# Kernel optimization log

Measured on AMD Instinct MI355X. Metric: run time of the kernel, lower is better.

The kernel has to match this reference:

```python
import jax, jax.numpy as jnp
import numpy as np

D = 512
H = 8
B, S = 4, 2048


def _layernorm(x, g, b, eps=1e-6):
    m = jnp.mean(x, axis=-1, keepdims=True)
    v = jnp.mean(jnp.square(x - m), axis=-1, keepdims=True)
    return (x - m) * jax.lax.rsqrt(v + eps) * g + b


def setup_inputs() -> dict:
    key = jax.random.key(0)
    ks = jax.random.split(key, 8)
    w = 1.0 / np.sqrt(D)  # glorot-ish scale so softmax doesn't saturate
    return {
        "x": jax.random.normal(ks[0], (B, S, D), dtype=jnp.float32),
        "Q": jax.random.normal(ks[1], (H, D, D), dtype=jnp.float32) * w,
        "K": jax.random.normal(ks[2], (H, D, D), dtype=jnp.float32) * w,
        "g1": jnp.ones((D,), jnp.float32),
        "beta1": jnp.zeros((D,), jnp.float32),
        "Wp": jax.random.normal(ks[3], (H * D, D), dtype=jnp.float32) / np.sqrt(H * D),
        "bp": jnp.zeros((D,), jnp.float32),
        "g2": jnp.ones((D,), jnp.float32),
        "beta2": jnp.zeros((D,), jnp.float32),
        "W1": jax.random.normal(ks[4], (D, 4 * D), dtype=jnp.float32) * w,
        "b1": jnp.zeros((4 * D,), jnp.float32),
        "W2": jax.random.normal(ks[5], (4 * D, D), dtype=jnp.float32) / np.sqrt(4 * D),
        "b2": jnp.zeros((D,), jnp.float32),
    }


def reference(x, Q, K, g1, beta1, Wp, bp, g2, beta2, W1, b1, W2, b2):
    # layernorm1
    xn = _layernorm(x, g1, beta1)  # [B,S,D]
    # per-head attention, batched over heads via einsum
    Qx = jnp.einsum("bsd,hde->hbse", xn, Q)  # [H,B,S,D]
    Kx = jnp.einsum("bsd,hde->hbse", xn, K)  # [H,B,S,D]
    scale = 1.0 / jnp.sqrt(jnp.float32(D))
    A = jnp.einsum("hbse,hbte->hbst", Qx, Kx) * scale  # [H,B,S,S]
    A = jax.nn.softmax(A, axis=-1)
    head = jnp.einsum("hbst,btd->hbsd", A, xn) + xn  # per-head residual
    # concat heads along last axis: order h0,h1,... -> [B,S,H*D]
    cat = jnp.transpose(head, (1, 2, 0, 3)).reshape(x.shape[0], x.shape[1], -1)
    # projection
    y = cat @ Wp + bp  # [B,S,D]
    # layernorm2
    y = _layernorm(y, g2, beta2)
    # MLP with residual, exact gelu (keras default)
    h = jax.nn.gelu(y @ W1 + b1, approximate=False)
    h = jax.nn.gelu(h @ W2 + b2, approximate=False)
    return y + h
```

## Files before the change

kernel.cpp:

```cpp
#include <hip/hip_runtime.h>

using u16 = unsigned short;
typedef u16 u16x8 __attribute__((ext_vector_type(8)));
typedef __bf16 bf16x8 __attribute__((ext_vector_type(8)));
typedef float f32x4 __attribute__((ext_vector_type(4)));

__device__ __forceinline__ u16 f2bf(float f) {
  unsigned u = __builtin_bit_cast(unsigned, f);
  u += 0x7fffu + ((u >> 16) & 1u);
  return (u16)(u >> 16);
}
__device__ __forceinline__ float bf2f(u16 h) {
  unsigned u = ((unsigned)h) << 16;
  return __builtin_bit_cast(float, u);
}
__device__ __forceinline__ f32x4 mfma16(u16x8 a, u16x8 b, f32x4 c) {
  return __builtin_amdgcn_mfma_f32_16x16x32_bf16(
      __builtin_bit_cast(bf16x8, a), __builtin_bit_cast(bf16x8, b), c, 0, 0, 0);
}
__device__ __forceinline__ float gelu_f(float v) {
  return 0.5f * v * (1.0f + erff(v * 0.70710678118654752f));
}
__device__ __forceinline__ void gll16(const u16* g, u16* l) {
  __builtin_amdgcn_global_load_lds(
      (const __attribute__((address_space(1))) unsigned*)g,
      (__attribute__((address_space(3))) unsigned*)l, 16, 0, 0);
}

__global__ void cast_kernel(const float* __restrict__ in, u16* __restrict__ out,
                            float scale) {
  const size_t i = ((size_t)blockIdx.x * 256 + threadIdx.x) * 4;
  float4 v = *(const float4*)(in + i);
  out[i] = f2bf(v.x * scale);
  out[i + 1] = f2bf(v.y * scale);
  out[i + 2] = f2bf(v.z * scale);
  out[i + 3] = f2bf(v.w * scale);
}

__device__ __forceinline__ float loadf(const float* p) { return *p; }
__device__ __forceinline__ float loadf(const u16* p) { return bf2f(*p); }

template <typename T>
__global__ void tcast_kernel(const T* __restrict__ in, u16* __restrict__ out, int R, int C,
                             float scale) {
  __shared__ float tile[32][33];
  const T* ip = in + (size_t)blockIdx.z * R * C;
  u16* op = out + (size_t)blockIdx.z * R * C;
  int c0 = blockIdx.x * 32, r0 = blockIdx.y * 32;
  int tx = threadIdx.x, ty = threadIdx.y;
#pragma unroll
  for (int i = 0; i < 32; i += 8)
    tile[ty + i][tx] = loadf(ip + (size_t)(r0 + ty + i) * C + (c0 + tx));
  __syncthreads();
#pragma unroll
  for (int i = 0; i < 32; i += 8)
    op[(size_t)(c0 + ty + i) * R + (r0 + tx)] = f2bf(tile[tx][ty + i] * scale);
}

__global__ void vtile_kernel(const u16* __restrict__ in, u16* __restrict__ out) {
  __shared__ u16 tile[32][33];
  const int b = blockIdx.z;
  const int d0 = blockIdx.x * 32, t0 = blockIdx.y * 32;
  const int tx = threadIdx.x, ty = threadIdx.y;
  const u16* ip = in + (size_t)b * 2048 * 512;
#pragma unroll
  for (int i = 0; i < 32; i += 8)
    tile[ty + i][tx] = ip[(size_t)(t0 + ty + i) * 512 + d0 + tx];
  __syncthreads();
  u16* op = out + ((size_t)b * 64 + (t0 >> 5)) * 16384;
#pragma unroll
  for (int i = 0; i < 32; i += 8) {
    const int d = d0 + ty + i;
    op[(size_t)(tx >> 3) * 4096 + (size_t)d * 8 + (tx & 7)] = tile[tx][ty + i];
  }
}

__global__ __launch_bounds__(256) void ln_kernel(
    const float* __restrict__ x, const float* __restrict__ x2,
    const float* __restrict__ g, const float* __restrict__ b,
    u16* __restrict__ obf, float* __restrict__ of32) {
  const int D = 512;
  int row = blockIdx.x;
  const float* xr = x + (size_t)row * D;
  float2 v = ((const float2*)xr)[threadIdx.x];
  if (x2 != nullptr) {
    float2 v2 = ((const float2*)(x2 + (size_t)row * D))[threadIdx.x];
    v.x += v2.x;
    v.y += v2.y;
  }
  float s = v.x + v.y;
#pragma unroll
  for (int o = 1; o < 64; o <<= 1) s += __shfl_xor(s, o);
  __shared__ float red[4];
  int wid = threadIdx.x >> 6;
  if ((threadIdx.x & 63) == 0) red[wid] = s;
  __syncthreads();
  float mean = (red[0] + red[1] + red[2] + red[3]) * (1.0f / D);
  float dx = v.x - mean, dy = v.y - mean;
  float q = dx * dx + dy * dy;
#pragma unroll
  for (int o = 1; o < 64; o <<= 1) q += __shfl_xor(q, o);
  __syncthreads();
  if ((threadIdx.x & 63) == 0) red[wid] = q;
  __syncthreads();
  float var = (red[0] + red[1] + red[2] + red[3]) * (1.0f / D);
  float rstd = rsqrtf(var + 1e-6f);
  int c = threadIdx.x * 2;
  float o0 = dx * rstd * g[c] + b[c];
  float o1 = dy * rstd * g[c + 1] + b[c + 1];
  obf[(size_t)row * D + c] = f2bf(o0);
  obf[(size_t)row * D + c + 1] = f2bf(o1);
  if (of32 != nullptr) {
    of32[(size_t)row * D + c] = o0;
    of32[(size_t)row * D + c + 1] = o1;
  }
}

__global__ __launch_bounds__(256) void gemm_kernel(
    const u16* __restrict__ A, const u16* __restrict__ Bt,
    const float* __restrict__ bias, const float* __restrict__ resid,
    void* __restrict__ Cout, int M, int N, int K, int ldB, int mode,
    size_t sA, size_t sB, size_t sC, size_t aHS) {
  __shared__ u16 As[128 * 64];
  __shared__ u16 Bs[128 * 64];
  A += (size_t)blockIdx.z * sA;
  Bt += (size_t)blockIdx.z * sB;
  const size_t zC = (size_t)blockIdx.z * sC;
  const int m0 = blockIdx.y * 128, n0 = blockIdx.x * 128;
  const int tid = threadIdx.x;
  const int l = tid & 63, wv = tid >> 6;
  const int wr = (wv >> 1) * 64, wc = (wv & 1) * 64;
  const int lr = l & 15, lq = l >> 4;
  const int srow = l >> 3;
  const int sc = l & 7;
  f32x4 z4 = {0.f, 0.f, 0.f, 0.f};
  f32x4 acc[4][4];
#pragma unroll
  for (int mi = 0; mi < 4; mi++)
#pragma unroll
    for (int ni = 0; ni < 4; ni++) acc[mi][ni] = z4;

  for (int k0 = 0; k0 < K; k0 += 64) {
    __syncthreads();
#pragma unroll
    for (int j = 0; j < 4; ++j) {
      const int r = wv * 32 + j * 8 + srow;
      const int kc = (sc ^ (r & 7)) * 8;
      const u16* asrc;
      if (aHS) asrc = A + (size_t)(k0 >> 9) * aHS + (size_t)(m0 + r) * 512 + ((k0 & 511) + kc);
      else asrc = A + (size_t)(m0 + r) * K + k0 + kc;
      gll16(asrc, &As[(wv * 32 + j * 8) * 64]);
      const u16* bsrc = Bt + (size_t)(n0 + r) * ldB + k0 + kc;
      gll16(bsrc, &Bs[(wv * 32 + j * 8) * 64]);
    }
    asm volatile("s_waitcnt vmcnt(0)" ::: "memory");
    __syncthreads();
#pragma unroll
    for (int kk = 0; kk < 2; ++kk) {
      const int rc = ((kk * 4 + lq) ^ (lr & 7)) * 8;
      u16x8 af[4], bfr[4];
#pragma unroll
      for (int mi = 0; mi < 4; mi++) af[mi] = *(const u16x8*)&As[(wr + mi * 16 + lr) * 64 + rc];
#pragma unroll
      for (int ni = 0; ni < 4; ni++) bfr[ni] = *(const u16x8*)&Bs[(wc + ni * 16 + lr) * 64 + rc];
#pragma unroll
      for (int mi = 0; mi < 4; mi++)
#pragma unroll
        for (int ni = 0; ni < 4; ni++) acc[mi][ni] = mfma16(af[mi], bfr[ni], acc[mi][ni]);
    }
  }
#pragma unroll
  for (int mi = 0; mi < 4; mi++) {
#pragma unroll
    for (int ni = 0; ni < 4; ni++) {
      const int gn = n0 + wc + ni * 16 + lr;
      const float bv = (mode != 0 && bias != nullptr && blockIdx.z == 0) ? bias[gn] : 0.0f;
#pragma unroll
      for (int r = 0; r < 4; r++) {
        const int gm = m0 + wr + mi * 16 + (l >> 4) * 4 + r;
        float v = acc[mi][ni][r];
        const size_t idx = zC + (size_t)gm * N + gn;
        if (mode == 0) ((u16*)Cout)[idx] = f2bf(v);
        else if (mode == 1) ((float*)Cout)[idx] = v + bv;
        else if (mode == 2) ((u16*)Cout)[idx] = f2bf(gelu_f(v + bv));
        else ((float*)Cout)[idx] = gelu_f(v + bv) + resid[(size_t)gm * N + gn];
      }
    }
  }
}

__global__ __launch_bounds__(512, 2) void flash_kernel(
    const u16* __restrict__ Qx, const u16* __restrict__ Kx,
    const u16* __restrict__ xnTt, const u16* __restrict__ xn,
    u16* __restrict__ headout) {
  __shared__ u16 Ks[2][32][512];
  __shared__ u16 Ps[128][40];
  __shared__ float fLds[128];
  __shared__ float lLds[128];

  const int tid = threadIdx.x;
  const int l = tid & 63, wv = tid >> 6;
  const int lr = l & 15, lq = l >> 4, lk8 = lq * 8;
  const int r7 = lr & 7;
  const int lin = blockIdx.y * gridDim.x + blockIdx.x;
  const int b = (lin & 7) >> 1;
  const int rem = (lin & 1) + (lin >> 3) * 2;
  const int h = rem & 7;
  const int s0 = (rem >> 3) * 128;
  const size_t rowHB = (size_t)h * 8192 + (size_t)b * 2048;
  const u16* Qbase = Qx + (rowHB + s0) * 512;
  const u16* Kbase = Kx + (size_t)b * 2048 * 512;
  const u16* Vbatch = xnTt + (size_t)b * 64 * 16384;
  const u16* xnb = xn + ((size_t)b * 2048 + s0) * 512;

  u16x8 q[16];
  {
    const u16* qr = Qbase + (size_t)(wv * 16 + lr) * 512 + lk8;
#pragma unroll
    for (int ks = 0; ks < 16; ks++) q[ks] = *(const u16x8*)(qr + ks * 32);
  }
  f32x4 z4 = {0.f, 0.f, 0.f, 0.f};
  f32x4 o[8][4];
#pragma unroll
  for (int mi = 0; mi < 8; mi++)
#pragma unroll
    for (int ni = 0; ni < 4; ni++) o[mi][ni] = z4;
  float m_r[4], l_r[4];
#pragma unroll
  for (int r = 0; r < 4; r++) { m_r[r] = -1e30f; l_r[r] = 0.f; }

#define STAGE(buf, tt0)                                                      \
  do {                                                                       \
    _Pragma("unroll") for (int j = 0; j < 4; ++j) {                          \
      const int row_ = wv * 4 + j;                                           \
      gll16(Kbase + (size_t)((tt0) + row_) * 512 + ((l ^ (row_ & 7)) * 8),   \
            &Ks[buf][row_][0]);                                              \
    }                                                                        \
  } while (0)

  STAGE(0, 0);
  for (int it = 0; it < 64; ++it) {
    const int cur = it & 1;
    asm volatile("s_waitcnt vmcnt(0)" ::: "memory");
    __builtin_amdgcn_s_barrier();
    __builtin_amdgcn_sched_barrier(0);
    STAGE(cur ^ 1, (size_t)((it + 1) & 63) * 32);
    __builtin_amdgcn_sched_barrier(0);
    f32x4 sv0 = z4, sv1 = z4;
    __builtin_amdgcn_s_setprio(1);
#pragma unroll
    for (int ks = 0; ks < 16; ks++) {
      const int col = (((ks << 2) | lq) ^ r7) << 3;
      u16x8 kb0 = *(const u16x8*)&Ks[cur][lr][col];
      u16x8 kb1 = *(const u16x8*)&Ks[cur][16 + lr][col];
      sv0 = mfma16(q[ks], kb0, sv0);
      sv1 = mfma16(q[ks], kb1, sv1);
    }
    __builtin_amdgcn_s_setprio(0);
    float tm[4], fac[4];
#pragma unroll
    for (int r = 0; r < 4; r++) tm[r] = fmaxf(sv0[r], sv1[r]);
#pragma unroll
    for (int r = 0; r < 4; r++) {
      tm[r] = fmaxf(tm[r], __shfl_xor(tm[r], 1));
      tm[r] = fmaxf(tm[r], __shfl_xor(tm[r], 2));
      tm[r] = fmaxf(tm[r], __shfl_xor(tm[r], 4));
      tm[r] = fmaxf(tm[r], __shfl_xor(tm[r], 8));
    }
#pragma unroll
    for (int r = 0; r < 4; r++) {
      float mn = fmaxf(m_r[r], tm[r]);
      fac[r] = __expf(m_r[r] - mn);
      m_r[r] = mn;
      float p0 = __expf(sv0[r] - mn);
      float p1 = __expf(sv1[r] - mn);
      const int prow = wv * 16 + lq * 4 + r;
      Ps[prow][lr] = f2bf(p0);
      Ps[prow][16 + lr] = f2bf(p1);
      float rs = p0 + p1;
      rs += __shfl_xor(rs, 1);
      rs += __shfl_xor(rs, 2);
      rs += __shfl_xor(rs, 4);
      rs += __shfl_xor(rs, 8);
      l_r[r] = l_r[r] * fac[r] + rs;
    }
    if (lr == 0) {
#pragma unroll
      for (int r = 0; r < 4; r++) fLds[wv * 16 + lq * 4 + r] = fac[r];
    }
    asm volatile("s_waitcnt lgkmcnt(0)" ::: "memory");
    __builtin_amdgcn_s_barrier();
    __builtin_amdgcn_sched_barrier(0);
    const u16* Vt_ = Vbatch + (size_t)it * 16384;
    u16x8 vb[4];
#pragma unroll
    for (int ni = 0; ni < 4; ni++)
      vb[ni] = *(const u16x8*)(Vt_ + lq * 4096 + (size_t)(wv * 64 + ni * 16 + lr) * 8);
    __builtin_amdgcn_sched_barrier(0);
#pragma unroll
    for (int mi = 0; mi < 8; mi++) {
#pragma unroll
      for (int r = 0; r < 4; r++) {
        const float fv = fLds[mi * 16 + lq * 4 + r];
#pragma unroll
        for (int ni = 0; ni < 4; ni++) o[mi][ni][r] *= fv;
      }
    }
    asm volatile("s_waitcnt vmcnt(4)" ::: "memory");
    __builtin_amdgcn_sched_barrier(0);
    __builtin_amdgcn_s_setprio(1);
#pragma unroll
    for (int mi = 0; mi < 8; mi++) {
      u16x8 pa = *(const u16x8*)&Ps[mi * 16 + lr][lk8];
#pragma unroll
      for (int ni = 0; ni < 4; ni++) o[mi][ni] = mfma16(pa, vb[ni], o[mi][ni]);
    }
    __builtin_amdgcn_s_setprio(0);
  }
#undef STAGE
  asm volatile("s_waitcnt vmcnt(0)" ::: "memory");
  if (lr == 0) {
#pragma unroll
    for (int r = 0; r < 4; r++) lLds[wv * 16 + lq * 4 + r] = l_r[r];
  }
  __syncthreads();
  u16* outp = headout + (rowHB + s0) * 512;
#pragma unroll
  for (int mi = 0; mi < 8; mi++) {
#pragma unroll
    for (int r = 0; r < 4; r++) {
      const int row = mi * 16 + lq * 4 + r;
      const float linv = 1.0f / lLds[row];
      const u16* xr = xnb + (size_t)row * 512;
      u16* orow = outp + (size_t)row * 512;
#pragma unroll
      for (int ni = 0; ni < 4; ni++) {
        const int c = wv * 64 + ni * 16 + lr;
        orow[c] = f2bf(o[mi][ni][r] * linv + bf2f(xr[c]));
      }
    }
  }
}

extern "C" void kernel_launch(void* const* d_in, const int* in_sizes, int n_in,
                              void* d_out, int out_size, void* d_ws, size_t ws_size,
                              hipStream_t stream) {
  (void)in_sizes; (void)n_in; (void)out_size; (void)ws_size;
  const float* x   = (const float*)d_in[0];
  const float* Qw  = (const float*)d_in[1];
  const float* Kw  = (const float*)d_in[2];
  const float* g1  = (const float*)d_in[3];
  const float* be1 = (const float*)d_in[4];
  const float* Wp  = (const float*)d_in[5];
  const float* bp  = (const float*)d_in[6];
  const float* g2  = (const float*)d_in[7];
  const float* be2 = (const float*)d_in[8];
  const float* W1  = (const float*)d_in[9];
  const float* b1  = (const float*)d_in[10];
  const float* W2  = (const float*)d_in[11];
  const float* b2  = (const float*)d_in[12];
  float* out = (float*)d_out;

  u16* ws = (u16*)d_ws;
  size_t off = 0;
  u16* Qc   = ws + off; off += 8ull * 512 * 512;
  u16* Kc   = ws + off; off += 8ull * 512 * 512;
  u16* Mht  = ws + off; off += 8ull * 512 * 512;
  u16* Wpt  = ws + off; off += 512ull * 4096;
  u16* W1t  = ws + off; off += 2048ull * 512;
  u16* W2t  = ws + off; off += 512ull * 2048;
  u16* xnb  = ws + off; off += 8192ull * 512;
  u16* xnTt = ws + off; off += 4ull * 512 * 2048;
  u16* Qx   = ws + off; off += 8ull * 8192 * 512;
  u16* yn   = ws + off; off += 8192ull * 512;
  float* y   = (float*)(ws + off); off += 8192ull * 512 * 4;
  float* ynf = (float*)(ws + off); off += 8192ull * 512 * 2;
  u16* h1 = Qx;

  const float qscale = 0.04419417382415922f;
  dim3 tb(32, 8);
  cast_kernel<<<2048, 256, 0, stream>>>(Qw, Qc, qscale);
  cast_kernel<<<2048, 256, 0, stream>>>(Kw, Kc, 1.0f);
  tcast_kernel<float><<<dim3(16, 128, 1), tb, 0, stream>>>(Wp, Wpt, 4096, 512, 1.0f);
  tcast_kernel<float><<<dim3(64, 16, 1), tb, 0, stream>>>(W1, W1t, 512, 2048, 1.0f);
  tcast_kernel<float><<<dim3(16, 64, 1), tb, 0, stream>>>(W2, W2t, 2048, 512, 1.0f);
  ln_kernel<<<8192, 256, 0, stream>>>(x, nullptr, g1, be1, xnb, nullptr);
  vtile_kernel<<<dim3(16, 64, 4), tb, 0, stream>>>(xnb, xnTt);
  gemm_kernel<<<dim3(4, 4, 8), 256, 0, stream>>>(Kc, Qc, nullptr, nullptr, Mht,
      512, 512, 512, 512, 0, 262144, 262144, 262144, 0);
  gemm_kernel<<<dim3(4, 64, 8), 256, 0, stream>>>(xnb, Mht, nullptr, nullptr, Qx,
      8192, 512, 512, 512, 0, 0, 262144, 4194304, 0);
  flash_kernel<<<dim3(16, 32), 512, 0, stream>>>(Qx, xnb, xnTt, xnb, Qx);
  gemm_kernel<<<dim3(4, 64, 2), 256, 0, stream>>>(Qx, Wpt, bp, nullptr, y,
      8192, 512, 2048, 4096, 1, 16777216, 2048, 4194304, 4194304);
  ln_kernel<<<8192, 256, 0, stream>>>(y, y + 4194304, g2, be2, yn, ynf);
  gemm_kernel<<<dim3(16, 64, 1), 256, 0, stream>>>(yn, W1t, b1, nullptr, h1,
      8192, 2048, 512, 512, 2, 0, 0, 0, 0);
  gemm_kernel<<<dim3(4, 64, 1), 256, 0, stream>>>(h1, W2t, b2, ynf, out,
      8192, 512, 2048, 2048, 3, 0, 0, 0, 0);
}
```

Baseline: 871.9 us.

## Restructure flash kernel so each wave owns full output rows across all columns

```diff
diff --git a/kernel.cpp b/kernel.cpp
--- a/kernel.cpp
+++ b/kernel.cpp
@@ -189,14 +189,12 @@
   }
 }
 
-__global__ __launch_bounds__(512, 2) void flash_kernel(
+__global__ __launch_bounds__(256, 1) void flash_kernel(
     const u16* __restrict__ Qx, const u16* __restrict__ Kx,
     const u16* __restrict__ xnTt, const u16* __restrict__ xn,
     u16* __restrict__ headout) {
   __shared__ u16 Ks[2][32][512];
-  __shared__ u16 Ps[128][40];
-  __shared__ float fLds[128];
-  __shared__ float lLds[128];
+  __shared__ u16 Pw[4][16][40];
 
   const int tid = threadIdx.x;
   const int l = tid & 63, wv = tid >> 6;
@@ -206,7 +204,7 @@
   const int b = (lin & 7) >> 1;
   const int rem = (lin & 1) + (lin >> 3) * 2;
   const int h = rem & 7;
-  const int s0 = (rem >> 3) * 128;
+  const int s0 = (rem >> 3) * 64;
   const size_t rowHB = (size_t)h * 8192 + (size_t)b * 2048;
   const u16* Qbase = Qx + (rowHB + s0) * 512;
   const u16* Kbase = Kx + (size_t)b * 2048 * 512;
@@ -220,19 +218,17 @@
     for (int ks = 0; ks < 16; ks++) q[ks] = *(const u16x8*)(qr + ks * 32);
   }
   f32x4 z4 = {0.f, 0.f, 0.f, 0.f};
-  f32x4 o[8][4];
-#pragma unroll
-  for (int mi = 0; mi < 8; mi++)
-#pragma unroll
-    for (int ni = 0; ni < 4; ni++) o[mi][ni] = z4;
+  f32x4 o[32];
+#pragma unroll
+  for (int ni = 0; ni < 32; ni++) o[ni] = z4;
   float m_r[4], l_r[4];
 #pragma unroll
   for (int r = 0; r < 4; r++) { m_r[r] = -1e30f; l_r[r] = 0.f; }
 
 #define STAGE(buf, tt0)                                                      \
   do {                                                                       \
-    _Pragma("unroll") for (int j = 0; j < 4; ++j) {                          \
-      const int row_ = wv * 4 + j;                                           \
+    _Pragma("unroll") for (int j = 0; j < 8; ++j) {                          \
+      const int row_ = wv * 8 + j;                                           \
       gll16(Kbase + (size_t)((tt0) + row_) * 512 + ((l ^ (row_ & 7)) * 8),   \
             &Ks[buf][row_][0]);                                              \
     }                                                                        \
@@ -243,6 +239,12 @@
     const int cur = it & 1;
     asm volatile("s_waitcnt vmcnt(0)" ::: "memory");
     __builtin_amdgcn_s_barrier();
+    __builtin_amdgcn_sched_barrier(0);
+    const u16* Vt_ = Vbatch + (size_t)it * 16384;
+    u16x8 vb[32];
+#pragma unroll
+    for (int ni = 0; ni < 32; ni++)
+      vb[ni] = *(const u16x8*)(Vt_ + lq * 4096 + (size_t)(ni * 16 + lr) * 8);
     __builtin_amdgcn_sched_barrier(0);
     STAGE(cur ^ 1, (size_t)((it + 1) & 63) * 32);
     __builtin_amdgcn_sched_barrier(0);
@@ -274,70 +276,50 @@
       m_r[r] = mn;
       float p0 = __expf(sv0[r] - mn);
       float p1 = __expf(sv1[r] - mn);
-      const int prow = wv * 16 + lq * 4 + r;
-      Ps[prow][lr] = f2bf(p0);
-      Ps[prow][16 + lr] = f2bf(p1);
-      float rs = p0 + p1;
-      rs += __shfl_xor(rs, 1);
-      rs += __shfl_xor(rs, 2);
-      rs += __shfl_xor(rs, 4);
-      rs += __shfl_xor(rs, 8);
-      l_r[r] = l_r[r] * fac[r] + rs;
-    }
-    if (lr == 0) {
-#pragma unroll
-      for (int r = 0; r < 4; r++) fLds[wv * 16 + lq * 4 + r] = fac[r];
+      Pw[wv][lq * 4 + r][lr] = f2bf(p0);
+      Pw[wv][lq * 4 + r][16 + lr] = f2bf(p1);
+      l_r[r] = l_r[r] * fac[r] + p0 + p1;
     }
     asm volatile("s_waitcnt lgkmcnt(0)" ::: "memory");
-    __builtin_amdgcn_s_barrier();
-    __builtin_amdgcn_sched_barrier(0);
-    const u16* Vt_ = Vbatch + (size_t)it * 16384;
-    u16x8 vb[4];
-#pragma unroll
-    for (int ni = 0; ni < 4; ni++)
-      vb[ni] = *(const u16x8*)(Vt_ + lq * 4096 + (size_t)(wv * 64 + ni * 16 + lr) * 8);
-    __builtin_amdgcn_sched_barrier(0);
-#pragma unroll
-    for (int mi = 0; mi < 8; mi++) {
-#pragma unroll
-      for (int r = 0; r < 4; r++) {
-        const float fv = fLds[mi * 16 + lq * 4 + r];
-#pragma unroll
-        for (int ni = 0; ni < 4; ni++) o[mi][ni][r] *= fv;
-      }
-    }
-    asm volatile("s_waitcnt vmcnt(4)" ::: "memory");
-    __builtin_amdgcn_sched_barrier(0);
+    __builtin_amdgcn_sched_barrier(0);
+#pragma unroll
+    for (int ni = 0; ni < 32; ni++) {
+#pragma unroll
+      for (int r = 0; r < 4; r++) o[ni][r] *= fac[r];
+    }
+    asm volatile("s_waitcnt vmcnt(8)" ::: "memory");
+    __builtin_amdgcn_sched_barrier(0);
+    u16x8 pa = *(const u16x8*)&Pw[wv][lr][lk8];
     __builtin_amdgcn_s_setprio(1);
 #pragma unroll
-    for (int mi = 0; mi < 8; mi++) {
-      u16x8 pa = *(const u16x8*)&Ps[mi * 16 + lr][lk8];
-#pragma unroll
-      for (int ni = 0; ni < 4; ni++) o[mi][ni] = mfma16(pa, vb[ni], o[mi][ni]);
+    for (int g = 0; g < 4; g++) {
+#pragma unroll
+      for (int j = 0; j < 8; j++) o[g * 8 + j] = mfma16(pa, vb[g * 8 + j], o[g * 8 + j]);
+      __builtin_amdgcn_sched_barrier(0);
     }
     __builtin_amdgcn_s_setprio(0);
   }
 #undef STAGE
   asm volatile("s_waitcnt vmcnt(0)" ::: "memory");
-  if (lr == 0) {
-#pragma unroll
-    for (int r = 0; r < 4; r++) lLds[wv * 16 + lq * 4 + r] = l_r[r];
-  }
-  __syncthreads();
+#pragma unroll
+  for (int r = 0; r < 4; r++) {
+    float s = l_r[r];
+    s += __shfl_xor(s, 1);
+    s += __shfl_xor(s, 2);
+    s += __shfl_xor(s, 4);
+    s += __shfl_xor(s, 8);
+    l_r[r] = 1.0f / s;
+  }
   u16* outp = headout + (rowHB + s0) * 512;
 #pragma unroll
-  for (int mi = 0; mi < 8; mi++) {
-#pragma unroll
-    for (int r = 0; r < 4; r++) {
-      const int row = mi * 16 + lq * 4 + r;
-      const float linv = 1.0f / lLds[row];
-      const u16* xr = xnb + (size_t)row * 512;
-      u16* orow = outp + (size_t)row * 512;
-#pragma unroll
-      for (int ni = 0; ni < 4; ni++) {
-        const int c = wv * 64 + ni * 16 + lr;
-        orow[c] = f2bf(o[mi][ni][r] * linv + bf2f(xr[c]));
-      }
+  for (int r = 0; r < 4; r++) {
+    const int row = wv * 16 + lq * 4 + r;
+    const u16* xr = xnb + (size_t)row * 512;
+    u16* orow = outp + (size_t)row * 512;
+#pragma unroll
+    for (int ni = 0; ni < 32; ni++) {
+      const int c = ni * 16 + lr;
+      orow[c] = f2bf(o[ni][r] * l_r[r] + bf2f(xr[c]));
     }
   }
 }
@@ -390,7 +372,7 @@
       512, 512, 512, 512, 0, 262144, 262144, 262144, 0);
   gemm_kernel<<<dim3(4, 64, 8), 256, 0, stream>>>(xnb, Mht, nullptr, nullptr, Qx,
       8192, 512, 512, 512, 0, 0, 262144, 4194304, 0);
-  flash_kernel<<<dim3(16, 32), 512, 0, stream>>>(Qx, xnb, xnTt, xnb, Qx);
+  flash_kernel<<<dim3(32, 32), 256, 0, stream>>>(Qx, xnb, xnTt, xnb, Qx);
   gemm_kernel<<<dim3(4, 64, 2), 256, 0, stream>>>(Qx, Wpt, bp, nullptr, y,
       8192, 512, 2048, 4096, 1, 16777216, 2048, 4194304, 4194304);
   ln_kernel<<<8192, 256, 0, stream>>>(y, y + 4194304, g2, be2, yn, ynf);
```

After: 2.085 ms. 139% more time.
